# Optimization experiments

Measured on AMD Instinct MI355X. Metric: run time of the kernel, lower is better.

## Reference

```python
import jax, jax.numpy as jnp
import numpy as np

DIM = 256
HEADS = 8
HEAD_DIM = DIM // HEADS          # 32 (v head dim, also defines scale)
QK_DIM = DIM // HEADS // 2       # 16 (q/k head dim)
SCALE = HEAD_DIM ** -0.5


def conv3x3(x, w, b):
    # x: [B,C,H,W], w: [O,I,3,3] (torch OIHW), padding=1 stride=1 == SAME
    y = jax.lax.conv_general_dilated(
        x, w, window_strides=(1, 1), padding='SAME',
        dimension_numbers=('NCHW', 'OIHW', 'NCHW'))
    return y + b[None, :, None, None]


def setup_inputs() -> dict:
    key = jax.random.key(0)
    ks = jax.random.split(key, 12)
    s = 0.02
    B, C, H, W = 1, DIM, 64, 64
    return {
        'x':       jax.random.normal(ks[0], (B, C, H, W), jnp.float32),
        'attn_kv': jax.random.normal(ks[1], (B, C, H, W), jnp.float32),
        'qw':  jax.random.normal(ks[2], (C, C, 3, 3), jnp.float32) * s,
        'qb':  jnp.zeros((C,), jnp.float32),
        'kvw': jax.random.normal(ks[3], (C, C, 3, 3), jnp.float32) * s,
        'kvb': jnp.zeros((C,), jnp.float32),
        'Wq':  jax.random.normal(ks[4], (C // 2, C), jnp.float32) * s,
        'bq':  jnp.zeros((C // 2,), jnp.float32),
        'Wk':  jax.random.normal(ks[5], (C // 2, C), jnp.float32) * s,
        'bk':  jnp.zeros((C // 2,), jnp.float32),
        'Wv':  jax.random.normal(ks[6], (C, C), jnp.float32) * s,
        'bv':  jnp.zeros((C,), jnp.float32),
        'Wp':  jax.random.normal(ks[7], (C, C), jnp.float32) * s,
        'bp':  jnp.zeros((C,), jnp.float32),
    }


def reference(x, attn_kv, qw, qb, kvw, kvb, Wq, bq, Wk, bk, Wv, bv, Wp, bp):
    B, C, Hh, Ww = x.shape
    N = Hh * Ww
    # conv projections
    xq = conv3x3(x, qw, qb)            # [B,C,H,W]
    kv = conv3x3(attn_kv, kvw, kvb)    # [B,C,H,W]
    # flatten to tokens [B,N,C]
    xf = xq.reshape(B, C, N).transpose(0, 2, 1)
    kvf = kv.reshape(B, C, N).transpose(0, 2, 1)
    # qkv projections with asymmetric head dims
    q = (xf @ Wq.T + bq).reshape(B, N, HEADS, QK_DIM).transpose(0, 2, 1, 3)    # [B,h,N,16]
    k = (kvf @ Wk.T + bk).reshape(B, N, HEADS, QK_DIM).transpose(0, 2, 1, 3)   # [B,h,N,16]
    v = (kvf @ Wv.T + bv).reshape(B, N, HEADS, HEAD_DIM).transpose(0, 2, 1, 3) # [B,h,N,32]
    # attention (manual softmax(q k^T) v)
    attn = jax.nn.softmax(jnp.einsum('bhnd,bhmd->bhnm', q * SCALE, k), axis=-1)  # [B,h,N,N]
    o = jnp.einsum('bhnm,bhmd->bhnd', attn, v)  # [B,h,N,32]
    # replicate the original transpose(1,2).reshape(B,N,C) on the [1,B,h,N,dv]
    # tensor: memory order becomes (h, B, N, dv) flattened into (B, N, C).
    o = jnp.transpose(o, (1, 0, 2, 3)).reshape(B, N, C)
    out = o @ Wp.T + bp                               # [B,N,C]
    return out.transpose(0, 2, 1).reshape(B, C, Hh, Ww)
```

## Files before the change

kernel.cpp:

```cpp
#include <hip/hip_runtime.h>

typedef unsigned short u16;
typedef __attribute__((ext_vector_type(8))) short bf16x8;
typedef __attribute__((ext_vector_type(4))) float f32x4;
typedef __attribute__((ext_vector_type(16))) float f32x16;
typedef __attribute__((ext_vector_type(4))) unsigned u32x4;
typedef __attribute__((ext_vector_type(2))) int i32x2;

struct alignas(8) u16x4 { u16 x, y, z, w; };

#define MFMA16(A, B, C) __builtin_amdgcn_mfma_f32_16x16x32_bf16(A, B, C, 0, 0, 0)
#define MFMA32(A, B, C) __builtin_amdgcn_mfma_f32_32x32x16_bf16(A, B, C, 0, 0, 0)
#define QSCALE (0.17677669529663689f * 1.4426950408889634f)

__device__ __forceinline__ u16 f2bf(float f) {
  unsigned u = __float_as_uint(f);
  u = (u + 0x7fffu + ((u >> 16) & 1u)) >> 16;
  return (u16)u;
}

__device__ __forceinline__ bf16x8 ldb8(const u16* p) {
  return *reinterpret_cast<const bf16x8*>(p);
}

__device__ __forceinline__ void glds16(const u16* g, u16* l) {
  __builtin_amdgcn_global_load_lds(
      (const __attribute__((address_space(1))) void*)g,
      (__attribute__((address_space(3))) void*)l, 16, 0, 0);
}

__global__ __launch_bounds__(256) void prep_kernel(
    const float* __restrict__ x, const float* __restrict__ akv,
    const float* __restrict__ qw, const float* __restrict__ kvw,
    const float* __restrict__ Wq, const float* __restrict__ Wk,
    const float* __restrict__ Wv, const float* __restrict__ Wp,
    u16* __restrict__ xpT, u16* __restrict__ w2,
    u16* __restrict__ wqs, u16* __restrict__ wks,
    u16* __restrict__ wvs, u16* __restrict__ wps)
{
  __shared__ float sm[64 * 65];
  const int b = blockIdx.x, t = threadIdx.x;
  if (b < 512) {
    const int z = b >> 8, rem = b & 255;
    const int cib = (rem >> 6) * 64, y = rem & 63;
    const float* in = (z ? akv : x);
    const int tc = t & 63, tr = t >> 6;
    #pragma unroll
    for (int i = 0; i < 16; ++i) {
      const int ci = i * 4 + tr;
      sm[ci * 65 + tc] = in[(size_t)(cib + ci) * 4096 + y * 64 + tc];
    }
    __syncthreads();
    u16* dst = xpT + (size_t)z * 4356 * 256;
    #pragma unroll
    for (int i = 0; i < 16; ++i) {
      const int px = i * 4 + tr;
      dst[(size_t)((y + 1) * 66 + px + 1) * 256 + cib + tc] = f2bf(sm[tc * 65 + px]);
    }
    return;
  }
  if (b < 642) {
    const int slot = (b - 512) * 4 + (t >> 6);
    const int z = slot >= 260 ? 1 : 0;
    const int j = slot - z * 260;
    int pos;
    if (j < 66) pos = j;
    else if (j < 132) pos = 65 * 66 + (j - 66);
    else { const int j2 = j - 132; pos = (1 + (j2 >> 1)) * 66 + (j2 & 1) * 65; }
    u16x4 zr = {0, 0, 0, 0};
    *reinterpret_cast<u16x4*>(xpT + (size_t)z * 4356 * 256 + (size_t)pos * 256 + (t & 63) * 4) = zr;
    return;
  }
  if (b < 1154) {
    const int idx = b - 642;
    const int z = idx >> 8, co = idx & 255;
    const float* src = (z ? kvw : qw) + (size_t)co * 2304;
    u16* dst = w2 + (size_t)z * 256 * 2304 + (size_t)co * 2304;
    #pragma unroll
    for (int i = 0; i < 9; ++i) sm[i * 256 + t] = src[i * 256 + t];
    __syncthreads();
    #pragma unroll
    for (int i = 0; i < 9; ++i) dst[i * 256 + t] = f2bf(sm[t * 9 + i]);
    return;
  }
  {
    int idx = (b - 1154) * 256 + t;
    if (idx < 32768) { wqs[idx] = f2bf(Wq[idx] * QSCALE); return; }
    idx -= 32768;
    if (idx < 32768) { wks[idx] = f2bf(Wk[idx]); return; }
    idx -= 32768;
    if (idx < 65536) { wvs[idx] = f2bf(Wv[idx]); return; }
    idx -= 65536;
    wps[idx] = f2bf(Wp[idx]);
  }
}

__global__ __launch_bounds__(256, 2) void conv_kernel(
    const u16* __restrict__ xpT, const u16* __restrict__ w2,
    const float* __restrict__ qb, const float* __restrict__ kvb,
    u16* __restrict__ xqt, u16* __restrict__ kvt)
{
  __shared__ u16 ab[3][64 * 64];
  __shared__ u16 bb[3][64 * 64];

  const int z = blockIdx.z;
  const u16* __restrict__ X = xpT + (size_t)z * 4356 * 256;
  const u16* __restrict__ W = w2 + (size_t)z * 256 * 2304;
  const float* bias = z ? kvb : qb;
  u16* out = z ? kvt : xqt;

  const int lane = threadIdx.x & 63, w = threadIdx.x >> 6;
  const int lo = lane & 15, g = lane >> 4;
  const int r8 = lane >> 3, c = lane & 7;
  const int wr = w >> 1, wc = w & 1;
  const int cobase = blockIdx.x * 64;
  const int tbase = blockIdx.y * 64;

  const bool isA = (w < 2);
  const u16* gb[4];
  int ldso[4];
  #pragma unroll
  for (int q = 0; q < 4; ++q) {
    const int flat = w * 4 + q;
    if (flat < 8) {
      const int j = flat;
      gb[q] = W + (size_t)(cobase + j * 8 + r8) * 2304 + (c ^ r8) * 8;
      ldso[q] = j * 512;
    } else {
      const int j = flat - 8;
      const int tok = tbase + j * 8 + r8;
      const int padrow = ((tok >> 6) + 1) * 66 + (tok & 63) + 1;
      gb[q] = X + (size_t)padrow * 256 + (c ^ r8) * 8;
      ldso[q] = j * 512;
    }
  }

  f32x4 acc[2][2] = {};

  auto stage = [&](int s, int bsel) {
    int srcoff;
    if (isA) {
      srcoff = s * 64;
    } else {
      const int kk = s >> 2;
      const int koff = (kk / 3 - 1) * 66 + (kk % 3) - 1;
      srcoff = koff * 256 + (s & 3) * 64;
    }
    u16* lb = isA ? ab[bsel] : bb[bsel];
    #pragma unroll
    for (int q = 0; q < 4; ++q)
      glds16(gb[q] + srcoff, lb + ldso[q]);
  };

  stage(0, 0);
  stage(1, 1);
  asm volatile("s_waitcnt vmcnt(4)" ::: "memory");
  __syncthreads();

  #pragma unroll 1
  for (int s = 0; s < 36; ++s) {
    const int cur = s % 3;
    if (s + 2 < 36) stage(s + 2, (s + 2) % 3);
    #pragma unroll
    for (int ks = 0; ks < 2; ++ks) {
      const int swz = ((ks * 4 + g) ^ (lo & 7)) * 8;
      const int rowA = wr * 32 + lo, colB = wc * 32 + lo;
      bf16x8 a0 = *reinterpret_cast<const bf16x8*>(&ab[cur][rowA * 64 + swz]);
      bf16x8 a1 = *reinterpret_cast<const bf16x8*>(&ab[cur][(rowA + 16) * 64 + swz]);
      bf16x8 b0 = *reinterpret_cast<const bf16x8*>(&bb[cur][colB * 64 + swz]);
      bf16x8 b1 = *reinterpret_cast<const bf16x8*>(&bb[cur][(colB + 16) * 64 + swz]);
      acc[0][0] = MFMA16(a0, b0, acc[0][0]);
      acc[0][1] = MFMA16(a0, b1, acc[0][1]);
      acc[1][0] = MFMA16(a1, b0, acc[1][0]);
      acc[1][1] = MFMA16(a1, b1, acc[1][1]);
    }
    if (s < 35) {
      if (s + 2 < 36) asm volatile("s_waitcnt vmcnt(4)" ::: "memory");
      else            asm volatile("s_waitcnt vmcnt(0)" ::: "memory");
      __syncthreads();
    }
  }

  #pragma unroll
  for (int af = 0; af < 2; ++af) {
    const int cb = cobase + wr * 32 + af * 16 + 4 * g;
    const float4 bi = *reinterpret_cast<const float4*>(bias + cb);
    #pragma unroll
    for (int bf = 0; bf < 2; ++bf) {
      const int t = tbase + wc * 32 + bf * 16 + lo;
      f32x4 v = acc[af][bf];
      u16x4 pk = { f2bf(v[0] + bi.x), f2bf(v[1] + bi.y),
                   f2bf(v[2] + bi.z), f2bf(v[3] + bi.w) };
      *reinterpret_cast<u16x4*>(out + (size_t)t * 256 + cb) = pk;
    }
  }
}

__global__ __launch_bounds__(256) void qkv_kernel(
    const u16* __restrict__ xqt, const u16* __restrict__ kvt,
    const u16* __restrict__ wqs, const u16* __restrict__ wks,
    const u16* __restrict__ wvs,
    const float* __restrict__ bq, const float* __restrict__ bk,
    const float* __restrict__ bv,
    u16* __restrict__ Qh, u16* __restrict__ Kh, u16* __restrict__ Vp)
{
  const int lane = threadIdx.x & 63, wid = threadIdx.x >> 6;
  const int lo = lane & 15, g = lane >> 4;
  const int bx = blockIdx.x;

  if (blockIdx.z == 0) {
    const bool isq = bx < 2;
    const u16* A = isq ? wqs : wks;
    const u16* Bm = isq ? xqt : kvt;
    const float* bias = isq ? bq : bk;
    const float bsc = isq ? (float)QSCALE : 1.f;
    u16* outp = isq ? Qh : Kh;
    const int c0 = (bx & 1) * 64 + (wid >> 1) * 32;
    const int n0 = blockIdx.y * 64 + (wid & 1) * 32;

    f32x4 acc[2][2] = {};
    #pragma unroll
    for (int s = 0; s < 8; ++s) {
      const int k0 = s * 32 + 8 * g;
      bf16x8 A0 = ldb8(A + (c0 + lo) * 256 + k0);
      bf16x8 A1 = ldb8(A + (c0 + 16 + lo) * 256 + k0);
      bf16x8 B0 = ldb8(Bm + (n0 + lo) * 256 + k0);
      bf16x8 B1 = ldb8(Bm + (n0 + 16 + lo) * 256 + k0);
      acc[0][0] = MFMA16(A0, B0, acc[0][0]);
      acc[0][1] = MFMA16(A0, B1, acc[0][1]);
      acc[1][0] = MFMA16(A1, B0, acc[1][0]);
      acc[1][1] = MFMA16(A1, B1, acc[1][1]);
    }
    #pragma unroll
    for (int af = 0; af < 2; ++af) {
      const int cb = c0 + af * 16 + 4 * g;
      const int h = cb >> 4, dd = cb & 15;
      const float4 bi = *reinterpret_cast<const float4*>(bias + cb);
      #pragma unroll
      for (int bfr = 0; bfr < 2; ++bfr) {
        const int n = n0 + bfr * 16 + lo;
        f32x4 v = acc[af][bfr];
        u16x4 pk = { f2bf(v[0] + bi.x * bsc), f2bf(v[1] + bi.y * bsc),
                     f2bf(v[2] + bi.z * bsc), f2bf(v[3] + bi.w * bsc) };
        *reinterpret_cast<u16x4*>(outp + h * 65536 + n * 16 + dd) = pk;
      }
    }
  } else {
    const int n0 = blockIdx.y * 64 + (wid >> 1) * 32;
    const int c0 = bx * 64 + (wid & 1) * 32;

    f32x4 acc[2][2] = {};
    #pragma unroll
    for (int s = 0; s < 8; ++s) {
      const int k0 = s * 32 + 8 * g;
      bf16x8 A0 = ldb8(kvt + (n0 + lo) * 256 + k0);
      bf16x8 A1 = ldb8(kvt + (n0 + 16 + lo) * 256 + k0);
      bf16x8 B0 = ldb8(wvs + (c0 + lo) * 256 + k0);
      bf16x8 B1 = ldb8(wvs + (c0 + 16 + lo) * 256 + k0);
      acc[0][0] = MFMA16(A0, B0, acc[0][0]);
      acc[0][1] = MFMA16(A0, B1, acc[0][1]);
      acc[1][0] = MFMA16(A1, B0, acc[1][0]);
      acc[1][1] = MFMA16(A1, B1, acc[1][1]);
    }
    #pragma unroll
    for (int af = 0; af < 2; ++af) {
      const int nb = n0 + af * 16 + 4 * g;
      const int tblk = nb >> 4, hhalf = (nb >> 3) & 1, j0 = nb & 7;
      #pragma unroll
      for (int bfr = 0; bfr < 2; ++bfr) {
        const int cc = c0 + bfr * 16 + lo;
        const int h = cc >> 5, dv = cc & 31;
        const float bi = bv[cc];
        f32x4 v = acc[af][bfr];
        u16x4 pk = { f2bf(v[0] + bi), f2bf(v[1] + bi),
                     f2bf(v[2] + bi), f2bf(v[3] + bi) };
        *reinterpret_cast<u16x4*>(
            Vp + (size_t)h * 131072 + tblk * 512 + hhalf * 256 + dv * 8 + j0) = pk;
      }
    }
  }
}

__global__ __launch_bounds__(512, 8) void attn_kernel(
    const u16* __restrict__ Qh, const u16* __restrict__ Kh,
    const u16* __restrict__ Vp, u16* __restrict__ O2)
{
  __shared__ float olds[16][8][64];
  __shared__ float l_lds[8][32];
  __shared__ float inv_lds[32];

  const int lane = threadIdx.x & 63, w = threadIdx.x >> 6;
  const int lo = lane & 31, hi = lane >> 5;
  const int h = blockIdx.y;
  const int qt0 = blockIdx.x * 32;

  const u16* Q = Qh + h * 65536;
  const u16* K = Kh + h * 65536;

  const bf16x8 qb = ldb8(Q + (qt0 + lo) * 16 + 8 * hi);

  f32x16 o = {0,0,0,0,0,0,0,0,0,0,0,0,0,0,0,0};
  float lacc0 = 0.f, lacc1 = 0.f;
  const int kvbase = w * 512;

  const u16* kptr = K + (kvbase + lo) * 16 + 8 * hi;
  const u16* vptr = Vp + (size_t)h * 131072 + (size_t)kvbase * 32 + lane * 8;

  #pragma unroll 1
  for (int st = 0; st < 16; ++st) {
    const bf16x8 kb = ldb8(kptr);
    const bf16x8 vb0 = ldb8(vptr);
    const bf16x8 vb1 = ldb8(vptr + 512);
    kptr += 512; vptr += 1024;

    const f32x16 zf = {0,0,0,0,0,0,0,0,0,0,0,0,0,0,0,0};
    f32x16 s = MFMA32(kb, qb, zf);

    unsigned cpk[8];
    #pragma unroll
    for (int r = 0; r < 16; r += 2) {
      const float p0 = __builtin_amdgcn_exp2f(s[r]);
      const float p1 = __builtin_amdgcn_exp2f(s[r + 1]);
      lacc0 += p0; lacc1 += p1;
      asm("v_cvt_pk_bf16_f32 %0, %1, %2" : "=v"(cpk[r >> 1]) : "v"(p0), "v"(p1));
    }

    u32x4 fa0, fa1;
    { i32x2 r2 = __builtin_amdgcn_permlane32_swap((int)cpk[0], (int)cpk[2], false, false);
      fa0[0] = (unsigned)r2[0]; fa0[2] = (unsigned)r2[1]; }
    { i32x2 r2 = __builtin_amdgcn_permlane32_swap((int)cpk[1], (int)cpk[3], false, false);
      fa0[1] = (unsigned)r2[0]; fa0[3] = (unsigned)r2[1]; }
    { i32x2 r2 = __builtin_amdgcn_permlane32_swap((int)cpk[4], (int)cpk[6], false, false);
      fa1[0] = (unsigned)r2[0]; fa1[2] = (unsigned)r2[1]; }
    { i32x2 r2 = __builtin_amdgcn_permlane32_swap((int)cpk[5], (int)cpk[7], false, false);
      fa1[1] = (unsigned)r2[0]; fa1[3] = (unsigned)r2[1]; }

    o = MFMA32(__builtin_bit_cast(bf16x8, fa0), vb0, o);
    o = MFMA32(__builtin_bit_cast(bf16x8, fa1), vb1, o);
  }

  float l = lacc0 + lacc1;
  l += __shfl_xor(l, 32);
  if (lane < 32) l_lds[w][lane] = l;
  #pragma unroll
  for (int r = 0; r < 16; ++r) olds[r][w][lane] = o[r];
  __syncthreads();

  if (w == 0 && lane < 32) {
    float L = 0.f;
    #pragma unroll
    for (int w2 = 0; w2 < 8; ++w2) L += l_lds[w2][lane];
    inv_lds[lane] = 1.0f / L;
  }
  __syncthreads();

  #pragma unroll
  for (int j = 0; j < 2; ++j) {
    const int r = 2 * w + j;
    const int q = (r & 3) + 8 * (r >> 2) + 4 * hi;
    float acc = 0.f;
    #pragma unroll
    for (int w2 = 0; w2 < 8; ++w2) acc += olds[r][w2][lane];
    acc *= inv_lds[q];
    const int n = qt0 + q;
    O2[(size_t)((h << 9) + (n >> 3)) * 256 + ((n & 7) << 5) + lo] = f2bf(acc);
  }
}

__global__ __launch_bounds__(256) void oproj_kernel(
    const u16* __restrict__ O2, const u16* __restrict__ wps,
    const float* __restrict__ bp, float* __restrict__ outp)
{
  const int lane = threadIdx.x & 63, wid = threadIdx.x >> 6;
  const int lo = lane & 15, g = lane >> 4;
  const int n0 = blockIdx.x * 64 + (wid >> 1) * 32;
  const int c0 = blockIdx.y * 64 + (wid & 1) * 32;

  f32x4 acc[2][2] = {};
  #pragma unroll
  for (int s = 0; s < 8; ++s) {
    const int k0 = s * 32 + 8 * g;
    bf16x8 A0 = ldb8(O2 + (n0 + lo) * 256 + k0);
    bf16x8 A1 = ldb8(O2 + (n0 + 16 + lo) * 256 + k0);
    bf16x8 B0 = ldb8(wps + (c0 + lo) * 256 + k0);
    bf16x8 B1 = ldb8(wps + (c0 + 16 + lo) * 256 + k0);
    acc[0][0] = MFMA16(A0, B0, acc[0][0]);
    acc[0][1] = MFMA16(A0, B1, acc[0][1]);
    acc[1][0] = MFMA16(A1, B0, acc[1][0]);
    acc[1][1] = MFMA16(A1, B1, acc[1][1]);
  }
  #pragma unroll
  for (int af = 0; af < 2; ++af) {
    const int nb = n0 + af * 16 + 4 * g;
    #pragma unroll
    for (int bfr = 0; bfr < 2; ++bfr) {
      const int c = c0 + bfr * 16 + lo;
      const float bi = bp[c];
      f32x4 v = acc[af][bfr];
      float4 r4;
      r4.x = v[0] + bi; r4.y = v[1] + bi; r4.z = v[2] + bi; r4.w = v[3] + bi;
      *reinterpret_cast<float4*>(outp + (size_t)c * 4096 + nb) = r4;
    }
  }
}

extern "C" void kernel_launch(void* const* d_in, const int* in_sizes, int n_in,
                              void* d_out, int out_size, void* d_ws, size_t ws_size,
                              hipStream_t stream) {
  (void)in_sizes; (void)n_in; (void)out_size; (void)ws_size;
  const float* x   = (const float*)d_in[0];
  const float* akv = (const float*)d_in[1];
  const float* qw  = (const float*)d_in[2];
  const float* qb  = (const float*)d_in[3];
  const float* kvw = (const float*)d_in[4];
  const float* kvb = (const float*)d_in[5];
  const float* Wq  = (const float*)d_in[6];
  const float* bq  = (const float*)d_in[7];
  const float* Wk  = (const float*)d_in[8];
  const float* bk  = (const float*)d_in[9];
  const float* Wv  = (const float*)d_in[10];
  const float* bv  = (const float*)d_in[11];
  const float* Wp  = (const float*)d_in[12];
  const float* bp  = (const float*)d_in[13];
  float* outp = (float*)d_out;

  char* wsb = (char*)d_ws;
  size_t off = 0;
  auto take = [&](size_t bytes) {
    char* p = wsb + off;
    off = (off + bytes + 255) & ~(size_t)255;
    return p;
  };
  u16* xpT = (u16*)take(2ULL * 4356 * 256 * 2);
  u16* w2  = (u16*)take(2ULL * 256 * 2304 * 2);
  u16* wqs = (u16*)take(128ULL * 256 * 2);
  u16* wks = (u16*)take(128ULL * 256 * 2);
  u16* wvs = (u16*)take(256ULL * 256 * 2);
  u16* wps = (u16*)take(256ULL * 256 * 2);
  u16* xqt = (u16*)take(4096ULL * 256 * 2);
  u16* kvt = (u16*)take(4096ULL * 256 * 2);
  u16* Qh  = (u16*)take(8ULL * 4096 * 16 * 2);
  u16* Kh  = (u16*)take(8ULL * 4096 * 16 * 2);
  u16* Vp  = (u16*)take(8ULL * 131072 * 2);
  u16* O2  = (u16*)take(4096ULL * 256 * 2);

  prep_kernel<<<dim3(1922), dim3(256), 0, stream>>>(
      x, akv, qw, kvw, Wq, Wk, Wv, Wp, xpT, w2, wqs, wks, wvs, wps);
  conv_kernel<<<dim3(4, 64, 2), dim3(256), 0, stream>>>(xpT, w2, qb, kvb, xqt, kvt);
  qkv_kernel<<<dim3(4, 64, 2), dim3(256), 0, stream>>>(
      xqt, kvt, wqs, wks, wvs, bq, bk, bv, Qh, Kh, Vp);
  attn_kernel<<<dim3(128, 8), dim3(512), 0, stream>>>(Qh, Kh, Vp, O2);
  oproj_kernel<<<dim3(64, 4), dim3(256), 0, stream>>>(O2, wps, bp, outp);
}
```

Measured before the change: 72.67 us.

## Process two query tiles per attention block to reuse K/V loads

Each attention block now handles 64 queries (two 32-query tiles) instead of 32, so every K and V fragment loaded from memory feeds two QK and PV MFMA chains. This halves K/V global traffic per query and doubles the independent work per iteration, giving more instruction-level parallelism. The grid is flattened so that heads are interleaved (h = bx & 7), which may change L2 locality. In exchange, register pressure rises (launch bounds relaxed from 8 to 4), the grid shrinks to 512 blocks, and the epilogue reduction runs twice with extra barriers.

```diff
diff --git a/kernel.cpp b/kernel.cpp
--- a/kernel.cpp
+++ b/kernel.cpp
@@ -281,26 +281,29 @@
   }
 }
 
-__global__ __launch_bounds__(512, 8) void attn_kernel(
+__global__ __launch_bounds__(512, 4) void attn_kernel(
     const u16* __restrict__ Qh, const u16* __restrict__ Kh,
     const u16* __restrict__ Vp, u16* __restrict__ O2)
 {
   __shared__ float olds[16][8][64];
-  __shared__ float l_lds[8][32];
-  __shared__ float inv_lds[32];
+  __shared__ float l_ldsA[8][32], l_ldsB[8][32];
+  __shared__ float invA[32], invB[32];
 
   const int lane = threadIdx.x & 63, w = threadIdx.x >> 6;
   const int lo = lane & 31, hi = lane >> 5;
-  const int h = blockIdx.y;
-  const int qt0 = blockIdx.x * 32;
+  const int bx = blockIdx.x;
+  const int h = bx & 7, qg = bx >> 3;
+  const int qt0 = qg * 64;
 
   const u16* Q = Qh + h * 65536;
   const u16* K = Kh + h * 65536;
 
-  const bf16x8 qb = ldb8(Q + (qt0 + lo) * 16 + 8 * hi);
-
-  f32x16 o = {0,0,0,0,0,0,0,0,0,0,0,0,0,0,0,0};
-  float lacc0 = 0.f, lacc1 = 0.f;
+  const bf16x8 qbA = ldb8(Q + (qt0 + lo) * 16 + 8 * hi);
+  const bf16x8 qbB = ldb8(Q + (qt0 + 32 + lo) * 16 + 8 * hi);
+
+  f32x16 oA = {0,0,0,0,0,0,0,0,0,0,0,0,0,0,0,0};
+  f32x16 oB = {0,0,0,0,0,0,0,0,0,0,0,0,0,0,0,0};
+  float lA0 = 0.f, lA1 = 0.f, lB0 = 0.f, lB1 = 0.f;
   const int kvbase = w * 512;
 
   const u16* kptr = K + (kvbase + lo) * 16 + 8 * hi;
@@ -314,43 +317,72 @@
     kptr += 512; vptr += 1024;
 
     const f32x16 zf = {0,0,0,0,0,0,0,0,0,0,0,0,0,0,0,0};
-    f32x16 s = MFMA32(kb, qb, zf);
-
-    unsigned cpk[8];
-    #pragma unroll
-    for (int r = 0; r < 16; r += 2) {
-      const float p0 = __builtin_amdgcn_exp2f(s[r]);
-      const float p1 = __builtin_amdgcn_exp2f(s[r + 1]);
-      lacc0 += p0; lacc1 += p1;
-      asm("v_cvt_pk_bf16_f32 %0, %1, %2" : "=v"(cpk[r >> 1]) : "v"(p0), "v"(p1));
-    }
-
-    u32x4 fa0, fa1;
-    { i32x2 r2 = __builtin_amdgcn_permlane32_swap((int)cpk[0], (int)cpk[2], false, false);
-      fa0[0] = (unsigned)r2[0]; fa0[2] = (unsigned)r2[1]; }
-    { i32x2 r2 = __builtin_amdgcn_permlane32_swap((int)cpk[1], (int)cpk[3], false, false);
-      fa0[1] = (unsigned)r2[0]; fa0[3] = (unsigned)r2[1]; }
-    { i32x2 r2 = __builtin_amdgcn_permlane32_swap((int)cpk[4], (int)cpk[6], false, false);
-      fa1[0] = (unsigned)r2[0]; fa1[2] = (unsigned)r2[1]; }
-    { i32x2 r2 = __builtin_amdgcn_permlane32_swap((int)cpk[5], (int)cpk[7], false, false);
-      fa1[1] = (unsigned)r2[0]; fa1[3] = (unsigned)r2[1]; }
-
-    o = MFMA32(__builtin_bit_cast(bf16x8, fa0), vb0, o);
-    o = MFMA32(__builtin_bit_cast(bf16x8, fa1), vb1, o);
-  }
-
-  float l = lacc0 + lacc1;
-  l += __shfl_xor(l, 32);
-  if (lane < 32) l_lds[w][lane] = l;
-  #pragma unroll
-  for (int r = 0; r < 16; ++r) olds[r][w][lane] = o[r];
+
+    {
+      f32x16 s = MFMA32(kb, qbA, zf);
+      unsigned cpk[8];
+      #pragma unroll
+      for (int r = 0; r < 16; r += 2) {
+        const float p0 = __builtin_amdgcn_exp2f(s[r]);
+        const float p1 = __builtin_amdgcn_exp2f(s[r + 1]);
+        lA0 += p0; lA1 += p1;
+        asm("v_cvt_pk_bf16_f32 %0, %1, %2" : "=v"(cpk[r >> 1]) : "v"(p0), "v"(p1));
+      }
+      u32x4 fa0, fa1;
+      { i32x2 r2 = __builtin_amdgcn_permlane32_swap((int)cpk[0], (int)cpk[2], false, false);
+        fa0[0] = (unsigned)r2[0]; fa0[2] = (unsigned)r2[1]; }
+      { i32x2 r2 = __builtin_amdgcn_permlane32_swap((int)cpk[1], (int)cpk[3], false, false);
+        fa0[1] = (unsigned)r2[0]; fa0[3] = (unsigned)r2[1]; }
+      { i32x2 r2 = __builtin_amdgcn_permlane32_swap((int)cpk[4], (int)cpk[6], false, false);
+        fa1[0] = (unsigned)r2[0]; fa1[2] = (unsigned)r2[1]; }
+      { i32x2 r2 = __builtin_amdgcn_permlane32_swap((int)cpk[5], (int)cpk[7], false, false);
+        fa1[1] = (unsigned)r2[0]; fa1[3] = (unsigned)r2[1]; }
+      oA = MFMA32(__builtin_bit_cast(bf16x8, fa0), vb0, oA);
+      oA = MFMA32(__builtin_bit_cast(bf16x8, fa1), vb1, oA);
+    }
+    {
+      f32x16 s = MFMA32(kb, qbB, zf);
+      unsigned cpk[8];
+      #pragma unroll
+      for (int r = 0; r < 16; r += 2) {
+        const float p0 = __builtin_amdgcn_exp2f(s[r]);
+        const float p1 = __builtin_amdgcn_exp2f(s[r + 1]);
+        lB0 += p0; lB1 += p1;
+        asm("v_cvt_pk_bf16_f32 %0, %1, %2" : "=v"(cpk[r >> 1]) : "v"(p0), "v"(p1));
+      }
+      u32x4 fa0, fa1;
+      { i32x2 r2 = __builtin_amdgcn_permlane32_swap((int)cpk[0], (int)cpk[2], false, false);
+        fa0[0] = (unsigned)r2[0]; fa0[2] = (unsigned)r2[1]; }
+      { i32x2 r2 = __builtin_amdgcn_permlane32_swap((int)cpk[1], (int)cpk[3], false, false);
+        fa0[1] = (unsigned)r2[0]; fa0[3] = (unsigned)r2[1]; }
+      { i32x2 r2 = __builtin_amdgcn_permlane32_swap((int)cpk[4], (int)cpk[6], false, false);
+        fa1[0] = (unsigned)r2[0]; fa1[2] = (unsigned)r2[1]; }
+      { i32x2 r2 = __builtin_amdgcn_permlane32_swap((int)cpk[5], (int)cpk[7], false, false);
+        fa1[1] = (unsigned)r2[0]; fa1[3] = (unsigned)r2[1]; }
+      oB = MFMA32(__builtin_bit_cast(bf16x8, fa0), vb0, oB);
+      oB = MFMA32(__builtin_bit_cast(bf16x8, fa1), vb1, oB);
+    }
+  }
+
+  float lA = lA0 + lA1;  lA += __shfl_xor(lA, 32);
+  float lB = lB0 + lB1;  lB += __shfl_xor(lB, 32);
+  if (lane < 32) { l_ldsA[w][lane] = lA; l_ldsB[w][lane] = lB; }
+
+  #pragma unroll
+  for (int r = 0; r < 16; ++r) olds[r][w][lane] = oA[r];
   __syncthreads();
 
   if (w == 0 && lane < 32) {
     float L = 0.f;
     #pragma unroll
-    for (int w2 = 0; w2 < 8; ++w2) L += l_lds[w2][lane];
-    inv_lds[lane] = 1.0f / L;
+    for (int w2 = 0; w2 < 8; ++w2) L += l_ldsA[w2][lane];
+    invA[lane] = 1.0f / L;
+  }
+  if (w == 1 && lane < 32) {
+    float L = 0.f;
+    #pragma unroll
+    for (int w2 = 0; w2 < 8; ++w2) L += l_ldsB[w2][lane];
+    invB[lane] = 1.0f / L;
   }
   __syncthreads();
 
@@ -361,8 +393,25 @@
     float acc = 0.f;
     #pragma unroll
     for (int w2 = 0; w2 < 8; ++w2) acc += olds[r][w2][lane];
-    acc *= inv_lds[q];
+    acc *= invA[q];
     const int n = qt0 + q;
+    O2[(size_t)((h << 9) + (n >> 3)) * 256 + ((n & 7) << 5) + lo] = f2bf(acc);
+  }
+  __syncthreads();
+
+  #pragma unroll
+  for (int r = 0; r < 16; ++r) olds[r][w][lane] = oB[r];
+  __syncthreads();
+
+  #pragma unroll
+  for (int j = 0; j < 2; ++j) {
+    const int r = 2 * w + j;
+    const int q = (r & 3) + 8 * (r >> 2) + 4 * hi;
+    float acc = 0.f;
+    #pragma unroll
+    for (int w2 = 0; w2 < 8; ++w2) acc += olds[r][w2][lane];
+    acc *= invB[q];
+    const int n = qt0 + 32 + q;
     O2[(size_t)((h << 9) + (n >> 3)) * 256 + ((n & 7) << 5) + lo] = f2bf(acc);
   }
 }
@@ -449,6 +498,6 @@
   conv_kernel<<<dim3(4, 64, 2), dim3(256), 0, stream>>>(xpT, w2, qb, kvb, xqt, kvt);
   qkv_kernel<<<dim3(4, 64, 2), dim3(256), 0, stream>>>(
       xqt, kvt, wqs, wks, wvs, bq, bk, bv, Qh, Kh, Vp);
-  attn_kernel<<<dim3(128, 8), dim3(512), 0, stream>>>(Qh, Kh, Vp, O2);
+  attn_kernel<<<dim3(512), dim3(512), 0, stream>>>(Qh, Kh, Vp, O2);
   oproj_kernel<<<dim3(64, 4), dim3(256), 0, stream>>>(O2, wps, bp, outp);
 }
```

Measured after the change: 70.05 us. 3.6% less time.
